# Kernel tuning notes

Measured on AMD Instinct MI355X. Metric: run time of the kernel, lower is better.

## Reference

```python
import jax, jax.numpy as jnp
import numpy as np

D_MODEL, D_QKV, N_HEADS = 1024, 64, 16


def setup_inputs() -> dict:
    key = jax.random.key(0)
    k_x, k_qkv, k_out = jax.random.split(key, 3)
    X = jax.random.normal(k_x, (2, 2048, D_MODEL), dtype=jnp.float32)
    # nn.Linear(d_model, 3*d_qkv*n_heads, bias=False): store as (in, out) for X @ W
    W_qkv = jax.random.normal(k_qkv, (D_MODEL, 3 * D_QKV * N_HEADS), dtype=jnp.float32) * (D_MODEL ** -0.5)
    W_out = jax.random.normal(k_out, (D_QKV * N_HEADS, D_MODEL), dtype=jnp.float32) * ((D_QKV * N_HEADS) ** -0.5)
    return {"X": X, "W_qkv": W_qkv, "W_out": W_out}


def reference(X, W_qkv, W_out):
    b, s, _ = X.shape
    h, d = N_HEADS, D_QKV
    scale = d ** 0.5
    qkv = X @ W_qkv                          # [b, s, 3*h*d]
    # Faithful to torch: view(b, s, h, d, 3).unbind(-1) -> interleaved q/k/v layout
    qkv = qkv.reshape(b, s, h, d, 3)
    q, k, v = qkv[..., 0], qkv[..., 1], qkv[..., 2]   # each [b, s, h, d]
    scores = jnp.einsum("bqhd,bkhd->bhqk", q, k) / scale
    weights = jax.nn.softmax(scores, axis=-1)          # [b, h, s, s]
    attn = jnp.einsum("bhqk,bkhd->bqhd", weights, v)   # [b, s, h, d]
    return attn.reshape(b, s, h * d) @ W_out           # [b, s, d_model]
```

## Files before the change

### kernel.cpp

```cpp
#include <hip/hip_runtime.h>
#include <hip/hip_bf16.h>
#include <math.h>

typedef __bf16 bf16;
typedef __bf16 bf16x4 __attribute__((ext_vector_type(4)));
typedef __bf16 bf16x8 __attribute__((ext_vector_type(8)));
typedef float f32x4 __attribute__((ext_vector_type(4)));

#define MFMA16(a, b, c) __builtin_amdgcn_mfma_f32_16x16x32_bf16(a, b, c, 0, 0, 0)

constexpr int D_MODEL = 1024;
constexpr int N_QKV   = 3072;
constexpr int BATCH   = 2;
constexpr int SEQ     = 2048;
constexpr int NH      = 16;
constexpr int DH      = 64;
constexpr int M_TOT   = BATCH * SEQ;

__device__ __forceinline__ void gl_lds16(const bf16* g, bf16* l) {
    __builtin_amdgcn_global_load_lds(
        (const __attribute__((address_space(1))) void*)g,
        (__attribute__((address_space(3))) void*)l, 16, 0, 0);
}

__device__ __forceinline__ void transpose_tile(
    const float* __restrict__ in, bf16* __restrict__ out,
    int K, int N, int n0, int k0, bf16 (*T)[72])
{
    const int tid = threadIdx.x;
    const int r   = tid >> 2;
    const int c4  = (tid & 3) * 16;

    const float* src = in + (size_t)(k0 + r) * N + n0 + c4;
    f32x4 v0 = *(const f32x4*)(src + 0);
    f32x4 v1 = *(const f32x4*)(src + 4);
    f32x4 v2 = *(const f32x4*)(src + 8);
    f32x4 v3 = *(const f32x4*)(src + 12);
    #pragma unroll
    for (int j = 0; j < 4; j++) {
        T[c4 + j][r]      = (bf16)v0[j];
        T[c4 + 4 + j][r]  = (bf16)v1[j];
        T[c4 + 8 + j][r]  = (bf16)v2[j];
        T[c4 + 12 + j][r] = (bf16)v3[j];
    }
    __syncthreads();
    bf16* dst = out + (size_t)(n0 + r) * K + k0 + c4;
    *(bf16x8*)(dst)     = *(const bf16x8*)&T[r][c4];
    *(bf16x8*)(dst + 8) = *(const bf16x8*)&T[r][c4 + 8];
}

__global__ __launch_bounds__(256) void prepass_kernel(
    const float* __restrict__ X, const float* __restrict__ Wqkv,
    const float* __restrict__ Wout,
    bf16* __restrict__ xb, bf16* __restrict__ wqkv_t, bf16* __restrict__ wout_t)
{
    __shared__ bf16 T[64][72];
    const int b = blockIdx.x;
    if (b < 2048) {
        const size_t i = ((size_t)b * 256 + threadIdx.x) * 8;
        f32x4 a0 = *(const f32x4*)(X + i);
        f32x4 a1 = *(const f32x4*)(X + i + 4);
        bf16x8 w;
        #pragma unroll
        for (int j = 0; j < 4; j++) { w[j] = (bf16)a0[j]; w[j + 4] = (bf16)a1[j]; }
        *(bf16x8*)(xb + i) = w;
    } else if (b < 2048 + 768) {
        const int idx = b - 2048;
        transpose_tile(Wqkv, wqkv_t, D_MODEL, N_QKV,
                       (idx % 48) * 64, (idx / 48) * 64, T);
    } else {
        const int idx = b - 2816;
        transpose_tile(Wout, wout_t, D_MODEL, D_MODEL,
                       (idx % 16) * 64, (idx / 16) * 64, T);
    }
}

__global__ __launch_bounds__(256) void qkv_gemm_kernel(
    const bf16* __restrict__ Xb, const bf16* __restrict__ Wt,
    bf16* __restrict__ qb, bf16* __restrict__ kb, bf16* __restrict__ vb)
{
    __shared__ __align__(16) bf16 As[128 * 64];
    __shared__ __align__(16) bf16 Bs[128 * 64];

    const int tid  = threadIdx.x;
    const int wave = tid >> 6;
    const int lane = tid & 63;
    const int quad = lane >> 4;
    const int l16  = lane & 15;
    const int sw   = l16 & 7;
    const int m0   = blockIdx.x * 128;
    const int n0   = blockIdx.y * 128;
    const int wm   = (wave & 1) * 64;
    const int wn   = (wave >> 1) * 64;

    const int srow = lane >> 3;
    const int sc_s = ((lane & 7) ^ srow) * 8;
    const int sc_d = (lane & 7) * 8;

    f32x4 acc[4][4];
    #pragma unroll
    for (int a = 0; a < 4; a++)
        #pragma unroll
        for (int b = 0; b < 4; b++) acc[a][b] = {0.f, 0.f, 0.f, 0.f};

    for (int kb0 = 0; kb0 < D_MODEL; kb0 += 64) {
        __syncthreads();
        #pragma unroll
        for (int j = 0; j < 4; j++) {
            const int row = wave * 32 + j * 8 + srow;
            gl_lds16(Xb + (size_t)(m0 + row) * D_MODEL + kb0 + sc_s,
                     As + row * 64 + sc_d);
            gl_lds16(Wt + (size_t)(n0 + row) * D_MODEL + kb0 + sc_s,
                     Bs + row * 64 + sc_d);
        }
        __syncthreads();

        #pragma unroll
        for (int ks = 0; ks < 2; ks++) {
            const int co = ((ks * 4 + quad) ^ sw) * 8;
            bf16x8 af[4], bfr[4];
            #pragma unroll
            for (int mi = 0; mi < 4; mi++)
                af[mi] = *(const bf16x8*)&As[(wm + mi * 16 + l16) * 64 + co];
            #pragma unroll
            for (int ni = 0; ni < 4; ni++)
                bfr[ni] = *(const bf16x8*)&Bs[(wn + ni * 16 + l16) * 64 + co];
            #pragma unroll
            for (int mi = 0; mi < 4; mi++)
                #pragma unroll
                for (int ni = 0; ni < 4; ni++)
                    acc[mi][ni] = MFMA16(af[mi], bfr[ni], acc[mi][ni]);
        }
    }

    #pragma unroll
    for (int ni = 0; ni < 4; ni++) {
        const int n     = n0 + wn + ni * 16 + l16;
        const int h     = n / 192;
        const int rem   = n - h * 192;
        const int d     = rem / 3;
        const int which = rem - d * 3;
        #pragma unroll
        for (int mi = 0; mi < 4; mi++) {
            const int row0 = m0 + wm + mi * 16 + quad * 4;
            const int b    = row0 >> 11;
            const int s0   = row0 & (SEQ - 1);
            const size_t bh = (size_t)(b * NH + h);
            if (which == 2) {
                bf16x4 pv;
                #pragma unroll
                for (int i = 0; i < 4; i++) pv[i] = (bf16)acc[mi][ni][i];
                *(bf16x4*)(vb + (bh * DH + d) * SEQ + s0) = pv;
            } else {
                bf16* dst = (which == 0) ? qb : kb;
                #pragma unroll
                for (int i = 0; i < 4; i++)
                    dst[(bh * SEQ + s0 + i) * DH + d] = (bf16)acc[mi][ni][i];
            }
        }
    }
}

__global__ __launch_bounds__(256) void attn_kernel(
    const bf16* __restrict__ qb, const bf16* __restrict__ kb,
    const bf16* __restrict__ vb, bf16* __restrict__ ob)
{
    __shared__ __align__(16) bf16 Ks[128 * 64];
    __shared__ __align__(16) bf16 Vt[64 * 128];
    __shared__ __align__(16) bf16 Ps[4][2][16][128];

    const int tid  = threadIdx.x;
    const int wave = tid >> 6;
    const int lane = tid & 63;
    const int quad = lane >> 4;
    const int l16  = lane & 15;
    const int sw   = l16 & 7;
    const int bh   = blockIdx.x;
    const int q0   = blockIdx.y * 128;
    const size_t base = (size_t)bh * SEQ * DH;

    bf16x8 qf[2][2];
    #pragma unroll
    for (int qs = 0; qs < 2; qs++) {
        const size_t qoff = base + (size_t)(q0 + wave * 32 + qs * 16 + l16) * DH + quad * 8;
        qf[qs][0] = *(const bf16x8*)(qb + qoff);
        qf[qs][1] = *(const bf16x8*)(qb + qoff + 32);
        #pragma unroll
        for (int j = 0; j < 8; j++) {
            qf[qs][0][j] = (bf16)((float)qf[qs][0][j] * 0.125f);
            qf[qs][1][j] = (bf16)((float)qf[qs][1][j] * 0.125f);
        }
    }

    bf16x8 ones;
    #pragma unroll
    for (int j = 0; j < 8; j++) ones[j] = (bf16)1.0f;

    f32x4 o_acc[2][4];
    f32x4 o_l[2] = {{0.f,0.f,0.f,0.f},{0.f,0.f,0.f,0.f}};
    #pragma unroll
    for (int qs = 0; qs < 2; qs++)
        #pragma unroll
        for (int t = 0; t < 4; t++) o_acc[qs][t] = {0.f, 0.f, 0.f, 0.f};

    for (int k0 = 0; k0 < SEQ; k0 += 128) {
        __syncthreads();
        #pragma unroll
        for (int j = 0; j < 4; j++) {
            const int o = j * 256 + tid;
            {
                const int r = o >> 3, c = (o & 7) ^ (r & 7);
                gl_lds16(kb + base + (size_t)(k0 + r) * DH + c * 8, Ks + o * 8);
            }
            {
                const int r = o >> 4, c = (o & 15) ^ (r & 7);
                gl_lds16(vb + base + (size_t)r * SEQ + k0 + c * 8, Vt + o * 8);
            }
        }
        __syncthreads();

        f32x4 sacc[2][8];
        #pragma unroll
        for (int qs = 0; qs < 2; qs++)
            #pragma unroll
            for (int t = 0; t < 8; t++) sacc[qs][t] = {0.f, 0.f, 0.f, 0.f};
        #pragma unroll
        for (int t = 0; t < 8; t++) {
            bf16x8 kf0 = *(const bf16x8*)&Ks[(t * 16 + l16) * 64 + ((quad)     ^ sw) * 8];
            bf16x8 kf1 = *(const bf16x8*)&Ks[(t * 16 + l16) * 64 + ((4 + quad) ^ sw) * 8];
            #pragma unroll
            for (int qs = 0; qs < 2; qs++) {
                sacc[qs][t] = MFMA16(kf0, qf[qs][0], sacc[qs][t]);
                sacc[qs][t] = MFMA16(kf1, qf[qs][1], sacc[qs][t]);
            }
        }

        #pragma unroll
        for (int qs = 0; qs < 2; qs++) {
            #pragma unroll
            for (int t = 0; t < 8; t++) {
                bf16x4 pv;
                #pragma unroll
                for (int i = 0; i < 4; i++)
                    pv[i] = (bf16)__expf(sacc[qs][t][i]);
                const int c2 = (2 * t + (quad >> 1)) ^ sw;
                *(bf16x4*)&Ps[wave][qs][l16][c2 * 8 + (quad & 1) * 4] = pv;
            }
        }

        #pragma unroll
        for (int ks = 0; ks < 4; ks++) {
            const int co = ((ks * 4 + quad) ^ sw) * 8;
            bf16x8 pf0 = *(const bf16x8*)&Ps[wave][0][l16][co];
            bf16x8 pf1 = *(const bf16x8*)&Ps[wave][1][l16][co];
            o_l[0] = MFMA16(pf0, ones, o_l[0]);
            o_l[1] = MFMA16(pf1, ones, o_l[1]);
            #pragma unroll
            for (int t = 0; t < 4; t++) {
                bf16x8 vf = *(const bf16x8*)&Vt[(t * 16 + l16) * 128 + co];
                o_acc[0][t] = MFMA16(pf0, vf, o_acc[0][t]);
                o_acc[1][t] = MFMA16(pf1, vf, o_acc[1][t]);
            }
        }
    }

    const int b = bh >> 4, h = bh & 15;
    #pragma unroll
    for (int qs = 0; qs < 2; qs++) {
        f32x4 linv;
        #pragma unroll
        for (int i = 0; i < 4; i++) linv[i] = 1.0f / o_l[qs][i];
        #pragma unroll
        for (int t = 0; t < 4; t++) {
            #pragma unroll
            for (int i = 0; i < 4; i++) {
                const int q = q0 + wave * 32 + qs * 16 + quad * 4 + i;
                ob[((size_t)(b * SEQ + q) * NH + h) * DH + t * 16 + l16] =
                    (bf16)(o_acc[qs][t][i] * linv[i]);
            }
        }
    }
}

__global__ __launch_bounds__(256) void out_gemm_kernel(
    const bf16* __restrict__ A, const bf16* __restrict__ Wt,
    float* __restrict__ out)
{
    __shared__ __align__(16) bf16 As[128 * 64];
    __shared__ __align__(16) bf16 Bs[128 * 64];

    const int tid  = threadIdx.x;
    const int wave = tid >> 6;
    const int lane = tid & 63;
    const int quad = lane >> 4;
    const int l16  = lane & 15;
    const int sw   = l16 & 7;
    const int m0   = blockIdx.x * 128;
    const int n0   = blockIdx.y * 128;
    const int wm   = (wave & 1) * 64;
    const int wn   = (wave >> 1) * 64;

    const int srow = lane >> 3;
    const int sc_s = ((lane & 7) ^ srow) * 8;
    const int sc_d = (lane & 7) * 8;

    f32x4 acc[4][4];
    #pragma unroll
    for (int a = 0; a < 4; a++)
        #pragma unroll
        for (int b = 0; b < 4; b++) acc[a][b] = {0.f, 0.f, 0.f, 0.f};

    for (int kb0 = 0; kb0 < D_MODEL; kb0 += 64) {
        __syncthreads();
        #pragma unroll
        for (int j = 0; j < 4; j++) {
            const int row = wave * 32 + j * 8 + srow;
            gl_lds16(A  + (size_t)(m0 + row) * D_MODEL + kb0 + sc_s,
                     As + row * 64 + sc_d);
            gl_lds16(Wt + (size_t)(n0 + row) * D_MODEL + kb0 + sc_s,
                     Bs + row * 64 + sc_d);
        }
        __syncthreads();

        #pragma unroll
        for (int ks = 0; ks < 2; ks++) {
            const int co = ((ks * 4 + quad) ^ sw) * 8;
            bf16x8 af[4], bfr[4];
            #pragma unroll
            for (int mi = 0; mi < 4; mi++)
                af[mi] = *(const bf16x8*)&As[(wm + mi * 16 + l16) * 64 + co];
            #pragma unroll
            for (int ni = 0; ni < 4; ni++)
                bfr[ni] = *(const bf16x8*)&Bs[(wn + ni * 16 + l16) * 64 + co];
            #pragma unroll
            for (int mi = 0; mi < 4; mi++)
                #pragma unroll
                for (int ni = 0; ni < 4; ni++)
                    acc[mi][ni] = MFMA16(af[mi], bfr[ni], acc[mi][ni]);
        }
    }

    #pragma unroll
    for (int mi = 0; mi < 4; mi++) {
        const int row0 = m0 + wm + mi * 16 + quad * 4;
        #pragma unroll
        for (int ni = 0; ni < 4; ni++) {
            const int n = n0 + wn + ni * 16 + l16;
            #pragma unroll
            for (int i = 0; i < 4; i++)
                out[(size_t)(row0 + i) * D_MODEL + n] = acc[mi][ni][i];
        }
    }
}

extern "C" void kernel_launch(void* const* d_in, const int* in_sizes, int n_in,
                              void* d_out, int out_size, void* d_ws, size_t ws_size,
                              hipStream_t stream)
{
    const float* X    = (const float*)d_in[0];
    const float* Wqkv = (const float*)d_in[1];
    const float* Wout = (const float*)d_in[2];
    float* out        = (float*)d_out;

    const size_t n_elem = (size_t)M_TOT * D_MODEL;
    bf16* qb      = (bf16*)d_ws;
    bf16* kb      = qb + n_elem;
    bf16* vb      = kb + n_elem;
    bf16* attnb   = vb + n_elem;
    bf16* wqkv_t  = attnb + n_elem;
    bf16* wout_t  = wqkv_t + (size_t)N_QKV * D_MODEL;
    bf16* xb      = wout_t + (size_t)D_MODEL * D_MODEL;

    prepass_kernel<<<3072, 256, 0, stream>>>(X, Wqkv, Wout, xb, wqkv_t, wout_t);

    qkv_gemm_kernel<<<dim3(M_TOT / 128, N_QKV / 128), 256, 0, stream>>>(
        xb, wqkv_t, qb, kb, vb);
    attn_kernel<<<dim3(BATCH * NH, SEQ / 128), 256, 0, stream>>>(qb, kb, vb, attnb);
    out_gemm_kernel<<<dim3(M_TOT / 128, D_MODEL / 128), 256, 0, stream>>>(
        attnb, wout_t, out);
}
```

Before: 197.2 us.

## Permute QKV weights to contiguous layout, load K/V directly from global, use exp2

Permutes the transposed QKV weight rows during the prepass so the GEMM epilogue computes q/k/v, head and dim with shifts instead of divisions. The attention kernel drops the shared-memory staging of K and V tiles and the two barriers per tile, reading fragments straight from global memory instead. It also folds log2(e) into the Q scale so softmax can use the hardware exp2. Direct global reads depend on cache hits, because every wave re-reads the same K/V data that LDS used to share across the block.

```diff
diff --git a/kernel.cpp b/kernel.cpp
--- a/kernel.cpp
+++ b/kernel.cpp
@@ -25,7 +25,7 @@
 
 __device__ __forceinline__ void transpose_tile(
     const float* __restrict__ in, bf16* __restrict__ out,
-    int K, int N, int n0, int k0, bf16 (*T)[72])
+    int K, int N, int n0, int k0, bf16 (*T)[72], bool permute)
 {
     const int tid = threadIdx.x;
     const int r   = tid >> 2;
@@ -44,7 +44,14 @@
         T[c4 + 12 + j][r] = (bf16)v3[j];
     }
     __syncthreads();
-    bf16* dst = out + (size_t)(n0 + r) * K + k0 + c4;
+    int rowg = n0 + r;
+    if (permute) {
+        const int which = rowg % 3;
+        const int h     = rowg / 192;
+        const int d     = (rowg % 192) / 3;
+        rowg = which * 1024 + h * 64 + d;
+    }
+    bf16* dst = out + (size_t)rowg * K + k0 + c4;
     *(bf16x8*)(dst)     = *(const bf16x8*)&T[r][c4];
     *(bf16x8*)(dst + 8) = *(const bf16x8*)&T[r][c4 + 8];
 }
@@ -67,11 +74,11 @@
     } else if (b < 2048 + 768) {
         const int idx = b - 2048;
         transpose_tile(Wqkv, wqkv_t, D_MODEL, N_QKV,
-                       (idx % 48) * 64, (idx / 48) * 64, T);
+                       (idx % 48) * 64, (idx / 48) * 64, T, true);
     } else {
         const int idx = b - 2816;
         transpose_tile(Wout, wout_t, D_MODEL, D_MODEL,
-                       (idx % 16) * 64, (idx / 16) * 64, T);
+                       (idx % 16) * 64, (idx / 16) * 64, T, false);
     }
 }
 
@@ -136,10 +143,9 @@
     #pragma unroll
     for (int ni = 0; ni < 4; ni++) {
         const int n     = n0 + wn + ni * 16 + l16;
-        const int h     = n / 192;
-        const int rem   = n - h * 192;
-        const int d     = rem / 3;
-        const int which = rem - d * 3;
+        const int which = n >> 10;
+        const int h     = (n >> 6) & 15;
+        const int d     = n & 63;
         #pragma unroll
         for (int mi = 0; mi < 4; mi++) {
             const int row0 = m0 + wm + mi * 16 + quad * 4;
@@ -165,8 +171,6 @@
     const bf16* __restrict__ qb, const bf16* __restrict__ kb,
     const bf16* __restrict__ vb, bf16* __restrict__ ob)
 {
-    __shared__ __align__(16) bf16 Ks[128 * 64];
-    __shared__ __align__(16) bf16 Vt[64 * 128];
     __shared__ __align__(16) bf16 Ps[4][2][16][128];
 
     const int tid  = threadIdx.x;
@@ -179,6 +183,7 @@
     const int q0   = blockIdx.y * 128;
     const size_t base = (size_t)bh * SEQ * DH;
 
+    constexpr float QSCALE = 0.125f * 1.44269504f;
     bf16x8 qf[2][2];
     #pragma unroll
     for (int qs = 0; qs < 2; qs++) {
@@ -187,8 +192,8 @@
         qf[qs][1] = *(const bf16x8*)(qb + qoff + 32);
         #pragma unroll
         for (int j = 0; j < 8; j++) {
-            qf[qs][0][j] = (bf16)((float)qf[qs][0][j] * 0.125f);
-            qf[qs][1][j] = (bf16)((float)qf[qs][1][j] * 0.125f);
+            qf[qs][0][j] = (bf16)((float)qf[qs][0][j] * QSCALE);
+            qf[qs][1][j] = (bf16)((float)qf[qs][1][j] * QSCALE);
         }
     }
 
@@ -203,22 +208,10 @@
         #pragma unroll
         for (int t = 0; t < 4; t++) o_acc[qs][t] = {0.f, 0.f, 0.f, 0.f};
 
+    const bf16* krow = kb + base;
+    const bf16* vrow = vb + base;
+
     for (int k0 = 0; k0 < SEQ; k0 += 128) {
-        __syncthreads();
-        #pragma unroll
-        for (int j = 0; j < 4; j++) {
-            const int o = j * 256 + tid;
-            {
-                const int r = o >> 3, c = (o & 7) ^ (r & 7);
-                gl_lds16(kb + base + (size_t)(k0 + r) * DH + c * 8, Ks + o * 8);
-            }
-            {
-                const int r = o >> 4, c = (o & 15) ^ (r & 7);
-                gl_lds16(vb + base + (size_t)r * SEQ + k0 + c * 8, Vt + o * 8);
-            }
-        }
-        __syncthreads();
-
         f32x4 sacc[2][8];
         #pragma unroll
         for (int qs = 0; qs < 2; qs++)
@@ -226,8 +219,9 @@
             for (int t = 0; t < 8; t++) sacc[qs][t] = {0.f, 0.f, 0.f, 0.f};
         #pragma unroll
         for (int t = 0; t < 8; t++) {
-            bf16x8 kf0 = *(const bf16x8*)&Ks[(t * 16 + l16) * 64 + ((quad)     ^ sw) * 8];
-            bf16x8 kf1 = *(const bf16x8*)&Ks[(t * 16 + l16) * 64 + ((4 + quad) ^ sw) * 8];
+            const bf16* kp = krow + (size_t)(k0 + t * 16 + l16) * DH + quad * 8;
+            bf16x8 kf0 = *(const bf16x8*)(kp);
+            bf16x8 kf1 = *(const bf16x8*)(kp + 32);
             #pragma unroll
             for (int qs = 0; qs < 2; qs++) {
                 sacc[qs][t] = MFMA16(kf0, qf[qs][0], sacc[qs][t]);
@@ -242,7 +236,7 @@
                 bf16x4 pv;
                 #pragma unroll
                 for (int i = 0; i < 4; i++)
-                    pv[i] = (bf16)__expf(sacc[qs][t][i]);
+                    pv[i] = (bf16)__builtin_amdgcn_exp2f(sacc[qs][t][i]);
                 const int c2 = (2 * t + (quad >> 1)) ^ sw;
                 *(bf16x4*)&Ps[wave][qs][l16][c2 * 8 + (quad & 1) * 4] = pv;
             }
@@ -257,7 +251,8 @@
             o_l[1] = MFMA16(pf1, ones, o_l[1]);
             #pragma unroll
             for (int t = 0; t < 4; t++) {
-                bf16x8 vf = *(const bf16x8*)&Vt[(t * 16 + l16) * 128 + co];
+                bf16x8 vf = *(const bf16x8*)(vrow + (size_t)(t * 16 + l16) * SEQ
+                                             + k0 + ks * 32 + quad * 8);
                 o_acc[0][t] = MFMA16(pf0, vf, o_acc[0][t]);
                 o_acc[1][t] = MFMA16(pf1, vf, o_acc[1][t]);
             }
```

After: 257.7 us. +30.7%, slower.
